# Kernel tuning notes

Hardware: AMD Instinct MI355X
Metric: run time of the kernel (lower is better)

The kernel has to match this reference:

```python
import jax, jax.numpy as jnp
import numpy as np

H = 8            # num_heads
EPS = 1e-5       # LayerNorm eps (torch default)
SLOPE = 0.01     # leaky_relu negative slope (torch default)


def layernorm(x, g, b):
    mu = jnp.mean(x, axis=-1, keepdims=True)
    var = jnp.mean((x - mu) ** 2, axis=-1, keepdims=True)
    return (x - mu) * jax.lax.rsqrt(var + EPS) * g + b


def setup_inputs() -> dict:
    key = jax.random.key(0)
    ks = jax.random.split(key, 20)
    B, T, Din, Dh = 4, 2048, 512, 512
    s_in = 1.0 / np.sqrt(Din)
    s_h = 1.0 / np.sqrt(Dh)
    inp = {
        'q': jax.random.normal(ks[0], (B, T, Din), jnp.float32),
        'k': jax.random.normal(ks[1], (B, T, Din), jnp.float32),
        'v': jax.random.normal(ks[2], (B, T, Din), jnp.float32),
        # attention projections (stored as [in, out] for x @ W + b)
        'Wq': jax.random.uniform(ks[3], (Din, Dh), jnp.float32, -s_in, s_in),
        'bq': jax.random.uniform(ks[4], (Dh,), jnp.float32, -s_in, s_in),
        'Wk': jax.random.uniform(ks[5], (Din, Dh), jnp.float32, -s_in, s_in),
        'bk': jax.random.uniform(ks[6], (Dh,), jnp.float32, -s_in, s_in),
        'Wv': jax.random.uniform(ks[7], (Din, Dh), jnp.float32, -s_in, s_in),
        'bv': jax.random.uniform(ks[8], (Dh,), jnp.float32, -s_in, s_in),
        'Wo': jax.random.uniform(ks[9], (Dh, Dh), jnp.float32, -s_h, s_h),
        'bo': jax.random.uniform(ks[10], (Dh,), jnp.float32, -s_h, s_h),
        # FFN
        'Wh': jax.random.uniform(ks[11], (Dh, Dh), jnp.float32, -s_h, s_h),
        'bh': jax.random.uniform(ks[12], (Dh,), jnp.float32, -s_h, s_h),
        'W2': jax.random.uniform(ks[13], (Dh, Dh), jnp.float32, -s_h, s_h),
        'b2': jax.random.uniform(ks[14], (Dh,), jnp.float32, -s_h, s_h),
        # LayerNorms
        'g1': jnp.ones((Dh,), jnp.float32),
        'be1': jnp.zeros((Dh,), jnp.float32),
        'g2': jnp.ones((Dh,), jnp.float32),
        'be2': jnp.zeros((Dh,), jnp.float32),
    }
    return inp


def _block(q, k, v, Wq, bq, Wk, bk, Wv, bv, Wo, bo, Wh, bh, W2, b2, g1, be1, g2, be2):
    B, Tq, _ = q.shape
    Tk = k.shape[1]
    Dh = Wq.shape[1]
    dh = Dh // H
    # projections -> [B, H, T, dh]
    qh = (q @ Wq + bq).reshape(B, Tq, H, dh).transpose(0, 2, 1, 3)
    kh = (k @ Wk + bk).reshape(B, Tk, H, dh).transpose(0, 2, 1, 3)
    vh = (v @ Wv + bv).reshape(B, Tk, H, dh).transpose(0, 2, 1, 3)
    scores = jnp.einsum('bhqd,bhkd->bhqk', qh, kh) / np.sqrt(dh)
    # causal mask: tril with diagonal = Tk - Tq (matches get_causal_mask)
    mask = jnp.tril(jnp.ones((Tq, Tk), bool), k=Tk - Tq)
    scores = jnp.where(mask, scores, -jnp.inf)
    attn = jax.nn.softmax(scores, axis=-1)
    x = jnp.einsum('bhqk,bhkd->bhqd', attn, vh)
    x = x.transpose(0, 2, 1, 3).reshape(B, Tq, Dh)
    h = x @ Wo + bo
    if h.shape == q.shape:
        h = h + q  # residual
    h = layernorm(h, g1, be1)
    y = jax.nn.leaky_relu(h @ Wh + bh, SLOPE) @ W2 + b2
    y = y + h  # residual (shapes always equal here)
    return layernorm(y, g2, be2)


def reference(q, k, v, Wq, bq, Wk, bk, Wv, bv, Wo, bo, Wh, bh, W2, b2, g1, be1, g2, be2):
    return _block(q, k, v, Wq, bq, Wk, bk, Wv, bv, Wo, bo, Wh, bh, W2, b2, g1, be1, g2, be2)
```

## Files before the change

kernel.cpp:

```cpp
#include <hip/hip_runtime.h>

#define DIN   512
#define TSEQ  2048
#define BATCH 4
#define NH    8
#define DHEAD 64
#define MTOT  8192

typedef __attribute__((ext_vector_type(8))) __bf16 bf16x8;
typedef __attribute__((ext_vector_type(8))) short  s16x8;
typedef __attribute__((ext_vector_type(4))) float  f32x4;

__device__ __forceinline__ unsigned short f2b(float f) {
  union { float f; unsigned int u; } c; c.f = f;
  unsigned int r = (c.u + 0x7fffu + ((c.u >> 16) & 1u)) >> 16;
  return (unsigned short)r;
}

__device__ __forceinline__ unsigned int pkbf(float a, float b) {
  union { __bf16 h[2]; unsigned int u; } c;
  c.h[0] = (__bf16)a; c.h[1] = (__bf16)b; return c.u;
}

__device__ __forceinline__ f32x4 mfma16(bf16x8 a, bf16x8 b, f32x4 c) {
  return __builtin_amdgcn_mfma_f32_16x16x32_bf16(a, b, c, 0, 0, 0);
}

__device__ __forceinline__ void gload16(const void* gsrc, void* ldsbase) {
  __builtin_amdgcn_global_load_lds(
      (const __attribute__((address_space(1))) unsigned int*)gsrc,
      (__attribute__((address_space(3))) unsigned int*)(unsigned int)(unsigned long long)ldsbase,
      16, 0, 0);
}

#define VMCNT0_BARRIER() do { \
    asm volatile("s_waitcnt vmcnt(0)" ::: "memory"); \
    __builtin_amdgcn_s_barrier(); } while (0)

__global__ __launch_bounds__(256) void cast3_kernel(const float* __restrict__ q,
                                                    const float* __restrict__ k,
                                                    const float* __restrict__ v,
                                                    unsigned short* __restrict__ oq,
                                                    unsigned short* __restrict__ ok,
                                                    unsigned short* __restrict__ ov) {
  const float* in = blockIdx.y == 0 ? q : blockIdx.y == 1 ? k : v;
  unsigned short* out = blockIdx.y == 0 ? oq : blockIdx.y == 1 ? ok : ov;
  int i = (blockIdx.x * 256 + threadIdx.x) * 8;
  float4 a = *(const float4*)(in + i);
  float4 b = *(const float4*)(in + i + 4);
  ushort4 u0, u1;
  u0.x = f2b(a.x); u0.y = f2b(a.y); u0.z = f2b(a.z); u0.w = f2b(a.w);
  u1.x = f2b(b.x); u1.y = f2b(b.y); u1.z = f2b(b.z); u1.w = f2b(b.w);
  *(ushort4*)(out + i) = u0;
  *(ushort4*)(out + i + 4) = u1;
}

__global__ __launch_bounds__(256) void transpose6_kernel(const float* __restrict__ w0,
                                                         const float* __restrict__ w1,
                                                         const float* __restrict__ w2,
                                                         const float* __restrict__ w3,
                                                         const float* __restrict__ w4,
                                                         const float* __restrict__ w5,
                                                         unsigned short* __restrict__ Wt) {
  const float* W;
  switch (blockIdx.z) {
    case 0: W = w0; break; case 1: W = w1; break; case 2: W = w2; break;
    case 3: W = w3; break; case 4: W = w4; break; default: W = w5; break;
  }
  unsigned short* dst = Wt + (size_t)blockIdx.z * 512 * 512;
  __shared__ float tile[32][33];
  int bx = blockIdx.x * 32, by = blockIdx.y * 32;
  int tx = threadIdx.x & 31, ty = threadIdx.x >> 5;
  #pragma unroll
  for (int yy = ty; yy < 32; yy += 8)
    tile[yy][tx] = W[(size_t)(by + yy) * DIN + bx + tx];
  __syncthreads();
  #pragma unroll
  for (int yy = ty; yy < 32; yy += 8)
    dst[(size_t)(bx + yy) * DIN + by + tx] = f2b(tile[tx][yy]);
}

__device__ __forceinline__ void gemm_core(const unsigned short* __restrict__ A,
                                          const unsigned short* __restrict__ Bt,
                                          int m0, int n0,
                                          unsigned short (*Als)[128 * 32],
                                          unsigned short (*Bls)[128 * 32],
                                          f32x4 (*acc)[4]) {
  const int tid = threadIdx.x, lane = tid & 63, w = tid >> 6;
  const int wr = w >> 1, wc = w & 1;
  const int l = lane & 15, g = lane >> 4;
  const int srow = lane >> 2;
  const int sce  = (lane & 3) * 8;

  #define STAGE(buf, k0) do { \
      _Pragma("unroll") \
      for (int i_ = 0; i_ < 2; ++i_) { \
        int ii_ = w * 2 + i_; \
        int row_ = ii_ * 16 + srow; \
        gload16(A  + (size_t)(m0 + row_) * 512 + (k0) + sce, &Als[buf][ii_ * 512]); \
        gload16(Bt + (size_t)(n0 + row_) * 512 + (k0) + sce, &Bls[buf][ii_ * 512]); \
      } } while (0)

  STAGE(0, 0);
  VMCNT0_BARRIER();
  for (int t = 0; t < 16; ++t) {
    int cur = t & 1;
    if (t < 15) STAGE(cur ^ 1, (t + 1) * 32);
    bf16x8 af[4], bf[4];
    #pragma unroll
    for (int m = 0; m < 4; ++m)
      af[m] = *(const bf16x8*)(&Als[cur][(wr * 64 + m * 16 + l) * 32 + g * 8]);
    #pragma unroll
    for (int n = 0; n < 4; ++n)
      bf[n] = *(const bf16x8*)(&Bls[cur][(wc * 64 + n * 16 + l) * 32 + g * 8]);
    #pragma unroll
    for (int m = 0; m < 4; ++m)
      #pragma unroll
      for (int n = 0; n < 4; ++n)
        acc[m][n] = mfma16(af[m], bf[n], acc[m][n]);
    VMCNT0_BARRIER();
  }
  #undef STAGE
}

enum { EPI_BF16 = 0, EPI_F32RES = 2, EPI_LRELU = 3 };

template <int EPI>
__global__ __launch_bounds__(256) void gemm_kernel(const unsigned short* __restrict__ A,
                                                   const unsigned short* __restrict__ Bt,
                                                   const float* __restrict__ bias,
                                                   const float* __restrict__ res,
                                                   void* __restrict__ out) {
  __shared__ unsigned short Als[2][128 * 32];
  __shared__ unsigned short Bls[2][128 * 32];
  const int lane = threadIdx.x & 63, w = threadIdx.x >> 6;
  const int wr = w >> 1, wc = w & 1;
  const int l = lane & 15, g = lane >> 4;
  const int m0 = blockIdx.x * 128, n0 = blockIdx.y * 128;
  f32x4 acc[4][4] = {};
  gemm_core(A, Bt, m0, n0, Als, Bls, acc);

  #pragma unroll
  for (int m = 0; m < 4; ++m) {
    int grb = m0 + wr * 64 + m * 16 + g * 4;
    #pragma unroll
    for (int n = 0; n < 4; ++n) {
      int gc = n0 + wc * 64 + n * 16 + l;
      float bv = bias[gc];
      #pragma unroll
      for (int r = 0; r < 4; ++r) {
        int gr = grb + r;
        float v = acc[m][n][r] + bv;
        if (EPI == EPI_F32RES) {
          ((float*)out)[(size_t)gr * 512 + gc] = v + res[(size_t)gr * 512 + gc];
        } else if (EPI == EPI_BF16) {
          ((unsigned short*)out)[(size_t)gr * 512 + gc] = f2b(v);
        } else {
          v = v > 0.f ? v : 0.01f * v;
          ((unsigned short*)out)[(size_t)gr * 512 + gc] = f2b(v);
        }
      }
    }
  }
}

__global__ __launch_bounds__(256) void gemm_qkv_kernel(const unsigned short* __restrict__ qb,
                                                       const unsigned short* __restrict__ kb,
                                                       const unsigned short* __restrict__ vb,
                                                       const unsigned short* __restrict__ Wt,
                                                       const float* __restrict__ bq,
                                                       const float* __restrict__ bk,
                                                       const float* __restrict__ bv,
                                                       unsigned short* __restrict__ Qp,
                                                       unsigned short* __restrict__ Kp,
                                                       unsigned short* __restrict__ Vt) {
  __shared__ unsigned short Als[2][128 * 32];
  __shared__ unsigned short Bls[2][128 * 32];
  const int z = blockIdx.z;
  const unsigned short* A = z == 0 ? qb : z == 1 ? kb : vb;
  const unsigned short* B = Wt + (size_t)z * 512 * 512;
  const float* bias = z == 0 ? bq : z == 1 ? bk : bv;
  const int lane = threadIdx.x & 63, w = threadIdx.x >> 6;
  const int wr = w >> 1, wc = w & 1;
  const int l = lane & 15, g = lane >> 4;
  const int m0 = blockIdx.x * 128, n0 = blockIdx.y * 128;
  f32x4 acc[4][4] = {};
  gemm_core(A, B, m0, n0, Als, Bls, acc);

  #pragma unroll
  for (int m = 0; m < 4; ++m) {
    int grb = m0 + wr * 64 + m * 16 + g * 4;
    #pragma unroll
    for (int n = 0; n < 4; ++n) {
      int gc = n0 + wc * 64 + n * 16 + l;
      float bvl = bias[gc];
      #pragma unroll
      for (int r = 0; r < 4; ++r) {
        int gr = grb + r;
        float v = acc[m][n][r] + bvl;
        if (z == 0) {
          Qp[(size_t)gr * 512 + gc] = f2b(v);
        } else if (z == 1) {
          Kp[(size_t)gr * 512 + gc] = f2b(v);
        } else {
          int b = gr >> 11, t = gr & 2047;
          Vt[((size_t)(b * 512 + gc) << 11) + t] = f2b(v);
        }
      }
    }
  }
}

__global__ __launch_bounds__(256) void attn_kernel(const unsigned short* __restrict__ Q,
                                                   const unsigned short* __restrict__ K,
                                                   const unsigned short* __restrict__ Vt,
                                                   unsigned short* __restrict__ O) {
  __shared__ unsigned short Kls[2][64 * 64];
  __shared__ unsigned short Vls[2][64 * 64];
  __shared__ unsigned short Pls[4][16 * 64];
  const int tid = threadIdx.x, lane = tid & 63, w = tid >> 6;
  const int l = lane & 15, g = lane >> 4;
  const int j = blockIdx.x;
  const int bh = blockIdx.y;
  const int b = bh >> 3, h = bh & 7;
  const int sx = (l & 7) * 8;
  const int n1 = 32 - j;

  const int r8 = lane >> 3;
  const int sce = ((lane & 7) ^ r8) * 8;

  #define STAGEKV(buf, kv0) do { \
      _Pragma("unroll") \
      for (int i_ = 0; i_ < 2; ++i_) { \
        int ii_ = w * 2 + i_; \
        int row_ = ii_ * 8 + r8; \
        gload16(K  + (size_t)(b * 2048 + (kv0) + row_) * 512 + h * 64 + sce, &Kls[buf][ii_ * 512]); \
        gload16(Vt + (size_t)(b * 512 + h * 64 + row_) * 2048 + (kv0) + sce, &Vls[buf][ii_ * 512]); \
      } } while (0)

  int tile = 31 - j;
  int q0 = tile * 64 + w * 16;
  bf16x8 qf[2];
  #pragma unroll
  for (int kf = 0; kf < 2; ++kf)
    qf[kf] = *(const bf16x8*)(Q + (size_t)(b * 2048 + q0 + l) * 512 + h * 64 + kf * 32 + g * 8);

  float mrun = -1e30f, lrun = 0.f;
  f32x4 o[4] = {};

  STAGEKV(0, 0);
  VMCNT0_BARRIER();

  for (int s = 0; s <= 32; ++s) {
    int cur = s & 1;
    int kb = s < n1 ? s : s - n1;
    int kv0 = kb * 64;
    if (s < 32) {
      int kbn = (s + 1) < n1 ? (s + 1) : (s + 1) - n1;
      STAGEKV(cur ^ 1, kbn * 64);
    }

    f32x4 st[4];
    #pragma unroll
    for (int t = 0; t < 4; ++t) {
      st[t] = f32x4{0.f, 0.f, 0.f, 0.f};
      #pragma unroll
      for (int kf = 0; kf < 2; ++kf) {
        bf16x8 kfr = *(const bf16x8*)(&Kls[cur][(t * 16 + l) * 64 + ((kf * 32 + g * 8) ^ sx)]);
        st[t] = mfma16(kfr, qf[kf], st[t]);
      }
    }
    const bool diag = (kb == tile);
    const int qrow = q0 + l;
    #pragma unroll
    for (int t = 0; t < 4; ++t)
      #pragma unroll
      for (int r = 0; r < 4; ++r) {
        float v = st[t][r] * 0.125f;
        if (diag && (kv0 + t * 16 + g * 4 + r > qrow)) v = -1e30f;
        st[t][r] = v;
      }

    float mx = fmaxf(fmaxf(fmaxf(st[0][0], st[0][1]), fmaxf(st[0][2], st[0][3])),
                     fmaxf(fmaxf(st[1][0], st[1][1]), fmaxf(st[1][2], st[1][3])));
    mx = fmaxf(mx, fmaxf(fmaxf(fmaxf(st[2][0], st[2][1]), fmaxf(st[2][2], st[2][3])),
                         fmaxf(fmaxf(st[3][0], st[3][1]), fmaxf(st[3][2], st[3][3]))));
    mx = fmaxf(mx, __shfl_xor(mx, 16, 64));
    mx = fmaxf(mx, __shfl_xor(mx, 32, 64));
    float nm = fmaxf(mrun, mx);
    float alpha = __expf(mrun - nm);
    mrun = nm;
    float rs = 0.f;
    #pragma unroll
    for (int t = 0; t < 4; ++t)
      #pragma unroll
      for (int r = 0; r < 4; ++r) {
        float p = __expf(st[t][r] - nm);
        st[t][r] = p;
        rs += p;
      }
    rs += __shfl_xor(rs, 16, 64);
    rs += __shfl_xor(rs, 32, 64);
    lrun = lrun * alpha + rs;

    #pragma unroll
    for (int r = 0; r < 4; ++r) {
      float ar = __shfl(alpha, g * 4 + r, 64);
      #pragma unroll
      for (int n = 0; n < 4; ++n) o[n][r] *= ar;
    }

    #pragma unroll
    for (int t = 0; t < 4; ++t) {
      uint2 u;
      u.x = pkbf(st[t][0], st[t][1]);
      u.y = pkbf(st[t][2], st[t][3]);
      *(uint2*)(&Pls[w][l * 64 + ((t * 16 + g * 4) ^ sx)]) = u;
    }
    #pragma unroll
    for (int kf = 0; kf < 2; ++kf) {
      bf16x8 pa = *(const bf16x8*)(&Pls[w][l * 64 + ((kf * 32 + g * 8) ^ sx)]);
      #pragma unroll
      for (int n = 0; n < 4; ++n) {
        bf16x8 vf = *(const bf16x8*)(&Vls[cur][(n * 16 + l) * 64 + ((kf * 32 + g * 8) ^ sx)]);
        o[n] = mfma16(pa, vf, o[n]);
      }
    }

    if (s == n1 - 1) {
      float li = 1.f / lrun;
      #pragma unroll
      for (int r = 0; r < 4; ++r) {
        float lir = __shfl(li, g * 4 + r, 64);
        #pragma unroll
        for (int n = 0; n < 4; ++n)
          O[(size_t)(b * 2048 + q0 + g * 4 + r) * 512 + h * 64 + n * 16 + l] =
              f2b(o[n][r] * lir);
      }
      tile = j;
      q0 = tile * 64 + w * 16;
      #pragma unroll
      for (int kf = 0; kf < 2; ++kf)
        qf[kf] = *(const bf16x8*)(Q + (size_t)(b * 2048 + q0 + l) * 512 + h * 64 + kf * 32 + g * 8);
      mrun = -1e30f; lrun = 0.f;
      #pragma unroll
      for (int n = 0; n < 4; ++n) o[n] = f32x4{0.f, 0.f, 0.f, 0.f};
    }
    VMCNT0_BARRIER();
  }

  float li = 1.f / lrun;
  #pragma unroll
  for (int r = 0; r < 4; ++r) {
    float lir = __shfl(li, g * 4 + r, 64);
    #pragma unroll
    for (int n = 0; n < 4; ++n)
      O[(size_t)(b * 2048 + q0 + g * 4 + r) * 512 + h * 64 + n * 16 + l] =
          f2b(o[n][r] * lir);
  }
  #undef STAGEKV
}

template <int WRITE_BF16>
__global__ __launch_bounds__(256) void ln_kernel(const float* __restrict__ X,
                                                 const float* __restrict__ g,
                                                 const float* __restrict__ be,
                                                 float* __restrict__ Yf,
                                                 unsigned short* __restrict__ Yb) {
  int row = blockIdx.x * 4 + (threadIdx.x >> 6);
  int lane = threadIdx.x & 63;
  const float* x = X + (size_t)row * 512;
  float4 v0 = *(const float4*)(x + lane * 4);
  float4 v1 = *(const float4*)(x + 256 + lane * 4);
  float s = v0.x + v0.y + v0.z + v0.w + v1.x + v1.y + v1.z + v1.w;
  #pragma unroll
  for (int t = 1; t < 64; t <<= 1) s += __shfl_xor(s, t, 64);
  float mu = s * (1.f / 512.f);
  float q = 0.f;
  q += (v0.x - mu) * (v0.x - mu); q += (v0.y - mu) * (v0.y - mu);
  q += (v0.z - mu) * (v0.z - mu); q += (v0.w - mu) * (v0.w - mu);
  q += (v1.x - mu) * (v1.x - mu); q += (v1.y - mu) * (v1.y - mu);
  q += (v1.z - mu) * (v1.z - mu); q += (v1.w - mu) * (v1.w - mu);
  #pragma unroll
  for (int t = 1; t < 64; t <<= 1) q += __shfl_xor(q, t, 64);
  float rstd = rsqrtf(q * (1.f / 512.f) + 1e-5f);

  float4 g0 = *(const float4*)(g + lane * 4);
  float4 g1 = *(const float4*)(g + 256 + lane * 4);
  float4 b0 = *(const float4*)(be + lane * 4);
  float4 b1 = *(const float4*)(be + 256 + lane * 4);
  float4 y0, y1;
  y0.x = (v0.x - mu) * rstd * g0.x + b0.x; y0.y = (v0.y - mu) * rstd * g0.y + b0.y;
  y0.z = (v0.z - mu) * rstd * g0.z + b0.z; y0.w = (v0.w - mu) * rstd * g0.w + b0.w;
  y1.x = (v1.x - mu) * rstd * g1.x + b1.x; y1.y = (v1.y - mu) * rstd * g1.y + b1.y;
  y1.z = (v1.z - mu) * rstd * g1.z + b1.z; y1.w = (v1.w - mu) * rstd * g1.w + b1.w;
  if (Yf) {
    *(float4*)(Yf + (size_t)row * 512 + lane * 4) = y0;
    *(float4*)(Yf + (size_t)row * 512 + 256 + lane * 4) = y1;
  }
  if (WRITE_BF16) {
    ushort4 u0, u1;
    u0.x = f2b(y0.x); u0.y = f2b(y0.y); u0.z = f2b(y0.z); u0.w = f2b(y0.w);
    u1.x = f2b(y1.x); u1.y = f2b(y1.y); u1.z = f2b(y1.z); u1.w = f2b(y1.w);
    *(ushort4*)(Yb + (size_t)row * 512 + lane * 4) = u0;
    *(ushort4*)(Yb + (size_t)row * 512 + 256 + lane * 4) = u1;
  }
}

extern "C" void kernel_launch(void* const* d_in, const int* in_sizes, int n_in,
                              void* d_out, int out_size, void* d_ws, size_t ws_size,
                              hipStream_t stream) {
  const float* q_in = (const float*)d_in[0];
  const float* k_in = (const float*)d_in[1];
  const float* v_in = (const float*)d_in[2];
  const float* Wq = (const float*)d_in[3];  const float* bq = (const float*)d_in[4];
  const float* Wk = (const float*)d_in[5];  const float* bk = (const float*)d_in[6];
  const float* Wv = (const float*)d_in[7];  const float* bv = (const float*)d_in[8];
  const float* Wo = (const float*)d_in[9];  const float* bo = (const float*)d_in[10];
  const float* Wh = (const float*)d_in[11]; const float* bh = (const float*)d_in[12];
  const float* W2 = (const float*)d_in[13]; const float* b2 = (const float*)d_in[14];
  const float* g1 = (const float*)d_in[15]; const float* be1 = (const float*)d_in[16];
  const float* g2 = (const float*)d_in[17]; const float* be2 = (const float*)d_in[18];

  char* ws = (char*)d_ws;
  const size_t MD2 = (size_t)MTOT * 512 * 2;
  const size_t W1  = (size_t)512 * 512 * 2;
  const size_t MD4 = (size_t)MTOT * 512 * 4;
  unsigned short* qb_  = (unsigned short*)(ws);
  unsigned short* kb_  = (unsigned short*)(ws + MD2);
  unsigned short* vb_  = (unsigned short*)(ws + 2 * MD2);
  unsigned short* Qp   = (unsigned short*)(ws + 3 * MD2);
  unsigned short* Kp   = (unsigned short*)(ws + 4 * MD2);
  unsigned short* Vt   = (unsigned short*)(ws + 5 * MD2);
  unsigned short* Wt   = (unsigned short*)(ws + 6 * MD2);
  float*          hy   = (float*)(ws + 6 * MD2 + 6 * W1);
  float*          ln1f = (float*)(ws + 6 * MD2 + 6 * W1 + MD4);
  unsigned short* attn = vb_;
  unsigned short* ln1b = qb_;
  unsigned short* f1   = kb_;

  cast3_kernel<<<dim3(MTOT * 512 / 2048, 3), 256, 0, stream>>>(q_in, k_in, v_in, qb_, kb_, vb_);
  transpose6_kernel<<<dim3(16, 16, 6), 256, 0, stream>>>(Wq, Wk, Wv, Wo, Wh, W2, Wt);

  gemm_qkv_kernel<<<dim3(MTOT / 128, 4, 3), 256, 0, stream>>>(
      qb_, kb_, vb_, Wt, bq, bk, bv, Qp, Kp, Vt);

  attn_kernel<<<dim3(16, BATCH * NH), 256, 0, stream>>>(Qp, Kp, Vt, attn);

  dim3 gg(MTOT / 128, 4);
  gemm_kernel<EPI_F32RES><<<gg, 256, 0, stream>>>(attn, Wt + 3 * 512 * 512, bo, q_in, hy);
  ln_kernel<1><<<MTOT / 4, 256, 0, stream>>>(hy, g1, be1, ln1f, ln1b);
  gemm_kernel<EPI_LRELU><<<gg, 256, 0, stream>>>(ln1b, Wt + 4 * 512 * 512, bh, nullptr, f1);
  gemm_kernel<EPI_F32RES><<<gg, 256, 0, stream>>>(f1, Wt + 5 * 512 * 512, b2, ln1f, hy);
  ln_kernel<0><<<MTOT / 4, 256, 0, stream>>>(hy, g2, be2, (float*)d_out, nullptr);
}
```

Measured before the change: 287.4 us.

## Retile GEMMs to 64x128 with BK=64 swizzled LDS; lazy softmax rescale in attention

The GEMM tile changes from 128x128 with a K-step of 32 to 64x128 with a K-step of 64, and an XOR swizzle is applied to the LDS layout. This doubles the number of blocks, giving better occupancy and wave count on the many CUs, and halves the number of barriers per K loop. In attention, the softmax scale is folded into exp2f via fmaf. The running-max rescale of O and l is skipped unless the new max exceeds the old one by a threshold, which saves multiplies and shuffles per KV tile. The risk is that exponent values can reach up to 2^(64*scale) before rescaling, which limits precision and overflow headroom.

New measurement: 258.9 us. -9.9%, faster.

```diff
diff --git a/kernel.cpp b/kernel.cpp
--- a/kernel.cpp
+++ b/kernel.cpp
@@ -1,4 +1,5 @@
 #include <hip/hip_runtime.h>
+#include <math.h>
 
 #define DIN   512
 #define TSEQ  2048
@@ -83,44 +84,51 @@
 __device__ __forceinline__ void gemm_core(const unsigned short* __restrict__ A,
                                           const unsigned short* __restrict__ Bt,
                                           int m0, int n0,
-                                          unsigned short (*Als)[128 * 32],
-                                          unsigned short (*Bls)[128 * 32],
+                                          unsigned short (*Als)[64 * 64],
+                                          unsigned short (*Bls)[128 * 64],
                                           f32x4 (*acc)[4]) {
   const int tid = threadIdx.x, lane = tid & 63, w = tid >> 6;
   const int wr = w >> 1, wc = w & 1;
   const int l = lane & 15, g = lane >> 4;
-  const int srow = lane >> 2;
-  const int sce  = (lane & 3) * 8;
-
-  #define STAGE(buf, k0) do { \
+  const int r8 = lane >> 3;
+  const int sce = ((lane & 7) ^ r8) * 8;
+  const int sxr = (l & 7) * 8;
+
+  #define GSTAGE(buf, k0) do { \
       _Pragma("unroll") \
       for (int i_ = 0; i_ < 2; ++i_) { \
-        int ii_ = w * 2 + i_; \
-        int row_ = ii_ * 16 + srow; \
-        gload16(A  + (size_t)(m0 + row_) * 512 + (k0) + sce, &Als[buf][ii_ * 512]); \
-        gload16(Bt + (size_t)(n0 + row_) * 512 + (k0) + sce, &Bls[buf][ii_ * 512]); \
+        int ia_ = w * 2 + i_; \
+        gload16(A + (size_t)(m0 + ia_ * 8 + r8) * 512 + (k0) + sce, &Als[buf][ia_ * 512]); \
+      } \
+      _Pragma("unroll") \
+      for (int i_ = 0; i_ < 4; ++i_) { \
+        int ib_ = w * 4 + i_; \
+        gload16(Bt + (size_t)(n0 + ib_ * 8 + r8) * 512 + (k0) + sce, &Bls[buf][ib_ * 512]); \
       } } while (0)
 
-  STAGE(0, 0);
+  GSTAGE(0, 0);
   VMCNT0_BARRIER();
-  for (int t = 0; t < 16; ++t) {
+  for (int t = 0; t < 8; ++t) {
     int cur = t & 1;
-    if (t < 15) STAGE(cur ^ 1, (t + 1) * 32);
-    bf16x8 af[4], bf[4];
-    #pragma unroll
-    for (int m = 0; m < 4; ++m)
-      af[m] = *(const bf16x8*)(&Als[cur][(wr * 64 + m * 16 + l) * 32 + g * 8]);
-    #pragma unroll
-    for (int n = 0; n < 4; ++n)
-      bf[n] = *(const bf16x8*)(&Bls[cur][(wc * 64 + n * 16 + l) * 32 + g * 8]);
-    #pragma unroll
-    for (int m = 0; m < 4; ++m)
+    if (t < 7) GSTAGE(cur ^ 1, (t + 1) * 64);
+    #pragma unroll
+    for (int kk = 0; kk < 2; ++kk) {
+      bf16x8 af[2], bf[4];
+      #pragma unroll
+      for (int m = 0; m < 2; ++m)
+        af[m] = *(const bf16x8*)(&Als[cur][(wr * 32 + m * 16 + l) * 64 + ((kk * 32 + g * 8) ^ sxr)]);
       #pragma unroll
       for (int n = 0; n < 4; ++n)
-        acc[m][n] = mfma16(af[m], bf[n], acc[m][n]);
+        bf[n] = *(const bf16x8*)(&Bls[cur][(wc * 64 + n * 16 + l) * 64 + ((kk * 32 + g * 8) ^ sxr)]);
+      #pragma unroll
+      for (int m = 0; m < 2; ++m)
+        #pragma unroll
+        for (int n = 0; n < 4; ++n)
+          acc[m][n] = mfma16(af[m], bf[n], acc[m][n]);
+    }
     VMCNT0_BARRIER();
   }
-  #undef STAGE
+  #undef GSTAGE
 }
 
 enum { EPI_BF16 = 0, EPI_F32RES = 2, EPI_LRELU = 3 };
@@ -131,18 +139,18 @@
                                                    const float* __restrict__ bias,
                                                    const float* __restrict__ res,
                                                    void* __restrict__ out) {
-  __shared__ unsigned short Als[2][128 * 32];
-  __shared__ unsigned short Bls[2][128 * 32];
+  __shared__ unsigned short Als[2][64 * 64];
+  __shared__ unsigned short Bls[2][128 * 64];
   const int lane = threadIdx.x & 63, w = threadIdx.x >> 6;
   const int wr = w >> 1, wc = w & 1;
   const int l = lane & 15, g = lane >> 4;
-  const int m0 = blockIdx.x * 128, n0 = blockIdx.y * 128;
-  f32x4 acc[4][4] = {};
+  const int m0 = blockIdx.x * 64, n0 = blockIdx.y * 128;
+  f32x4 acc[2][4] = {};
   gemm_core(A, Bt, m0, n0, Als, Bls, acc);
 
   #pragma unroll
-  for (int m = 0; m < 4; ++m) {
-    int grb = m0 + wr * 64 + m * 16 + g * 4;
+  for (int m = 0; m < 2; ++m) {
+    int grb = m0 + wr * 32 + m * 16 + g * 4;
     #pragma unroll
     for (int n = 0; n < 4; ++n) {
       int gc = n0 + wc * 64 + n * 16 + l;
@@ -174,8 +182,8 @@
                                                        unsigned short* __restrict__ Qp,
                                                        unsigned short* __restrict__ Kp,
                                                        unsigned short* __restrict__ Vt) {
-  __shared__ unsigned short Als[2][128 * 32];
-  __shared__ unsigned short Bls[2][128 * 32];
+  __shared__ unsigned short Als[2][64 * 64];
+  __shared__ unsigned short Bls[2][128 * 64];
   const int z = blockIdx.z;
   const unsigned short* A = z == 0 ? qb : z == 1 ? kb : vb;
   const unsigned short* B = Wt + (size_t)z * 512 * 512;
@@ -183,13 +191,13 @@
   const int lane = threadIdx.x & 63, w = threadIdx.x >> 6;
   const int wr = w >> 1, wc = w & 1;
   const int l = lane & 15, g = lane >> 4;
-  const int m0 = blockIdx.x * 128, n0 = blockIdx.y * 128;
-  f32x4 acc[4][4] = {};
+  const int m0 = blockIdx.x * 64, n0 = blockIdx.y * 128;
+  f32x4 acc[2][4] = {};
   gemm_core(A, B, m0, n0, Als, Bls, acc);
 
   #pragma unroll
-  for (int m = 0; m < 4; ++m) {
-    int grb = m0 + wr * 64 + m * 16 + g * 4;
+  for (int m = 0; m < 2; ++m) {
+    int grb = m0 + wr * 32 + m * 16 + g * 4;
     #pragma unroll
     for (int n = 0; n < 4; ++n) {
       int gc = n0 + wc * 64 + n * 16 + l;
@@ -225,6 +233,8 @@
   const int b = bh >> 3, h = bh & 7;
   const int sx = (l & 7) * 8;
   const int n1 = 32 - j;
+  const float SC2 = 0.125f * 1.44269504088896340736f;
+  const float THR = 64.f;
 
   const int r8 = lane >> 3;
   const int sce = ((lane & 7) ^ r8) * 8;
@@ -270,16 +280,14 @@
         st[t] = mfma16(kfr, qf[kf], st[t]);
       }
     }
-    const bool diag = (kb == tile);
-    const int qrow = q0 + l;
-    #pragma unroll
-    for (int t = 0; t < 4; ++t)
-      #pragma unroll
-      for (int r = 0; r < 4; ++r) {
-        float v = st[t][r] * 0.125f;
-        if (diag && (kv0 + t * 16 + g * 4 + r > qrow)) v = -1e30f;
-        st[t][r] = v;
-      }
+    if (kb == tile) {
+      const int qrow = q0 + l;
+      #pragma unroll
+      for (int t = 0; t < 4; ++t)
+        #pragma unroll
+        for (int r = 0; r < 4; ++r)
+          if (kv0 + t * 16 + g * 4 + r > qrow) st[t][r] = -1e30f;
+    }
 
     float mx = fmaxf(fmaxf(fmaxf(st[0][0], st[0][1]), fmaxf(st[0][2], st[0][3])),
                      fmaxf(fmaxf(st[1][0], st[1][1]), fmaxf(st[1][2], st[1][3])));
@@ -287,28 +295,33 @@
                          fmaxf(fmaxf(st[3][0], st[3][1]), fmaxf(st[3][2], st[3][3]))));
     mx = fmaxf(mx, __shfl_xor(mx, 16, 64));
     mx = fmaxf(mx, __shfl_xor(mx, 32, 64));
-    float nm = fmaxf(mrun, mx);
-    float alpha = __expf(mrun - nm);
-    mrun = nm;
+
+    if (!__all(mx <= mrun + THR)) {
+      float nm = fmaxf(mrun, mx);
+      float alpha = exp2f((mrun - nm) * SC2);
+      mrun = nm;
+      lrun *= alpha;
+      #pragma unroll
+      for (int r = 0; r < 4; ++r) {
+        float ar = __shfl(alpha, g * 4 + r, 64);
+        #pragma unroll
+        for (int n = 0; n < 4; ++n) o[n][r] *= ar;
+      }
+    }
+
+    float mS = mrun * SC2;
     float rs = 0.f;
     #pragma unroll
     for (int t = 0; t < 4; ++t)
       #pragma unroll
       for (int r = 0; r < 4; ++r) {
-        float p = __expf(st[t][r] - nm);
+        float p = exp2f(fmaf(st[t][r], SC2, -mS));
         st[t][r] = p;
         rs += p;
       }
     rs += __shfl_xor(rs, 16, 64);
     rs += __shfl_xor(rs, 32, 64);
-    lrun = lrun * alpha + rs;
-
-    #pragma unroll
-    for (int r = 0; r < 4; ++r) {
-      float ar = __shfl(alpha, g * 4 + r, 64);
-      #pragma unroll
-      for (int n = 0; n < 4; ++n) o[n][r] *= ar;
-    }
+    lrun += rs;
 
     #pragma unroll
     for (int t = 0; t < 4; ++t) {
@@ -442,12 +455,12 @@
   cast3_kernel<<<dim3(MTOT * 512 / 2048, 3), 256, 0, stream>>>(q_in, k_in, v_in, qb_, kb_, vb_);
   transpose6_kernel<<<dim3(16, 16, 6), 256, 0, stream>>>(Wq, Wk, Wv, Wo, Wh, W2, Wt);
 
-  gemm_qkv_kernel<<<dim3(MTOT / 128, 4, 3), 256, 0, stream>>>(
+  gemm_qkv_kernel<<<dim3(MTOT / 64, 4, 3), 256, 0, stream>>>(
       qb_, kb_, vb_, Wt, bq, bk, bv, Qp, Kp, Vt);
 
   attn_kernel<<<dim3(16, BATCH * NH), 256, 0, stream>>>(Qp, Kp, Vt, attn);
 
-  dim3 gg(MTOT / 128, 4);
+  dim3 gg(MTOT / 64, 4);
   gemm_kernel<EPI_F32RES><<<gg, 256, 0, stream>>>(attn, Wt + 3 * 512 * 512, bo, q_in, hy);
   ln_kernel<1><<<MTOT / 4, 256, 0, stream>>>(hy, g1, be1, ln1f, ln1b);
   gemm_kernel<EPI_LRELU><<<gg, 256, 0, stream>>>(ln1b, Wt + 4 * 512 * 512, bh, nullptr, f1);
```
